# Kernel tuning notes

Measured on AMD Instinct MI355X. Metric: run time of the kernel, lower is better.

The kernel has to match this reference:

```python
import jax, jax.numpy as jnp
import numpy as np

NUM_EXPERTS = 8
CAPACITY_C = 1.0
ROUTER_TEMP = 1.0
EPS = 1e-10


def reference(x, router_w, router_b, w_gate, b_gate, w_up, b_up, w_down, b_down):
    # x: [B, S, H]
    B, S, H = x.shape
    n_tok = B * S
    k = int(n_tok * CAPACITY_C) // NUM_EXPERTS  # expert capacity (1024 here)

    xf = x.reshape(n_tok, H)  # (b s) h

    # Linear router (dropout p=0 -> identity), computed in float32 as in .float()
    clean_h = xf @ router_w + router_b  # [n_tok, E]

    # Gumbel noise (deterministic key stands in for torch.rand_like)
    u = jax.random.uniform(jax.random.key(42), clean_h.shape, dtype=clean_h.dtype)
    gumbel = -jnp.log(-jnp.log(u + EPS) + EPS)
    h = (clean_h + gumbel) / ROUTER_TEMP

    Sm = jax.nn.softmax(h, axis=-1)  # softmax over experts

    # top-k over the TOKEN dim (dim=0) per expert -> expert-choice routing
    Gt, idxt = jax.lax.top_k(Sm.T, k)  # [E, k]
    G = Gt.T            # [k, E] routing weights
    idx = idxt.T        # [k, E] chosen token indices

    # Gather routed tokens (replaces the one-hot einsum gather exactly:
    # top-k indices are distinct per expert, so one-hot matmul == take)
    toks = jnp.take(xf, idx, axis=0)  # [k, E, H]

    # Shared SwiGLU FFN (group_size=1 -> one expert instance reused E times)
    gate = jax.nn.silu(toks @ w_gate + b_gate)  # [k, E, dff]
    up = toks @ w_up + b_up                      # [k, E, dff]
    e_out = (gate * up) @ w_down + b_down        # [k, E, H]

    # Weight by G and scatter-add back to token positions, summed over experts
    weighted = G[..., None] * e_out              # [k, E, H]
    y = jnp.zeros_like(xf).at[idx.reshape(-1)].add(weighted.reshape(-1, H))
    return y.reshape(B, S, H)


def setup_inputs() -> dict:
    key = jax.random.key(0)
    ks = jax.random.split(key, 6)
    B, S, H, E = 4, 2048, 2048, NUM_EXPERTS
    dff = int(H * 4 * 2 / 3)  # 5461
    sH = 1.0 / np.sqrt(H)
    sF = 1.0 / np.sqrt(dff)
    return {
        "x": jax.random.normal(ks[0], (B, S, H), dtype=jnp.float32),
        "router_w": jax.random.normal(ks[1], (H, E), dtype=jnp.float32) * sH,
        "router_b": jnp.zeros((E,), dtype=jnp.float32),
        "w_gate": jax.random.normal(ks[2], (H, dff), dtype=jnp.float32) * sH,
        "b_gate": jnp.zeros((dff,), dtype=jnp.float32),
        "w_up": jax.random.normal(ks[3], (H, dff), dtype=jnp.float32) * sH,
        "b_up": jnp.zeros((dff,), dtype=jnp.float32),
        "w_down": jax.random.normal(ks[4], (dff, H), dtype=jnp.float32) * sF,
        "b_down": jnp.zeros((H,), dtype=jnp.float32),
    }
```

## Files before the change

### kernel.cpp

```cpp
#include <hip/hip_runtime.h>
#include <cstdint>
#include <cstddef>

#define N_TOK  8192
#define HDIM   2048
#define NEXP   8
#define KCAP   1024
#define DFF    5461
#define DFF_PB 5504
#define ACT_P  5504
#define NT1    (HDIM / 64)
#define NT2    (ACT_P / 64)

typedef unsigned short u16;
typedef short bf16x8 __attribute__((ext_vector_type(8)));
typedef float f32x4  __attribute__((ext_vector_type(4)));

__device__ __forceinline__ u16 f2bf(float f) {
  uint32_t u = __float_as_uint(f);
  uint32_t r = (u + 0x7FFFu + ((u >> 16) & 1u)) >> 16;
  return (u16)r;
}

__device__ __forceinline__ uint32_t rotl32(uint32_t v, int d) {
  return (v << d) | (v >> (32 - d));
}

__device__ uint32_t threefry_bits(uint32_t idx) {
  const uint32_t ks0 = 0u, ks1 = 42u, ks2 = 0u ^ 42u ^ 0x1BD11BDAu;
  uint32_t x0 = 0u + ks0;
  uint32_t x1 = idx + ks1;
#define TFR(d) { x0 += x1; x1 = rotl32(x1, d); x1 ^= x0; }
  TFR(13) TFR(15) TFR(26) TFR(6)
  x0 += ks1; x1 += ks2 + 1u;
  TFR(17) TFR(29) TFR(16) TFR(24)
  x0 += ks2; x1 += ks0 + 2u;
  TFR(13) TFR(15) TFR(26) TFR(6)
  x0 += ks0; x1 += ks1 + 3u;
  TFR(17) TFR(29) TFR(16) TFR(24)
  x0 += ks1; x1 += ks2 + 4u;
  TFR(13) TFR(15) TFR(26) TFR(6)
  x0 += ks2; x1 += ks0 + 5u;
#undef TFR
  return x0 ^ x1;
}

__global__ __launch_bounds__(256) void router_kernel(const float* __restrict__ x,
    const float* __restrict__ rw, const float* __restrict__ rb,
    float* __restrict__ SmT)
{
  const int lane = threadIdx.x & 63;
  const int wid  = threadIdx.x >> 6;
  const int t = blockIdx.x * 4 + wid;
  const float* xr = x + (size_t)t * HDIM;
  float acc[8] = {0.f,0.f,0.f,0.f,0.f,0.f,0.f,0.f};
#pragma unroll
  for (int it = 0; it < HDIM / 64; ++it) {
    int h = lane + it * 64;
    float xv = xr[h];
    const float4* wp = (const float4*)(rw + h * 8);
    float4 w0 = wp[0], w1 = wp[1];
    acc[0] = fmaf(xv, w0.x, acc[0]);
    acc[1] = fmaf(xv, w0.y, acc[1]);
    acc[2] = fmaf(xv, w0.z, acc[2]);
    acc[3] = fmaf(xv, w0.w, acc[3]);
    acc[4] = fmaf(xv, w1.x, acc[4]);
    acc[5] = fmaf(xv, w1.y, acc[5]);
    acc[6] = fmaf(xv, w1.z, acc[6]);
    acc[7] = fmaf(xv, w1.w, acc[7]);
  }
#pragma unroll
  for (int m = 32; m >= 1; m >>= 1) {
#pragma unroll
    for (int e = 0; e < 8; ++e) acc[e] += __shfl_xor(acc[e], m, 64);
  }
  if (lane == 0) {
    float h[8];
#pragma unroll
    for (int e = 0; e < 8; ++e) {
      uint32_t bits = threefry_bits((uint32_t)(t * 8 + e));
      float u = __uint_as_float((bits >> 9) | 0x3f800000u) - 1.0f;
      u = fmaxf(u, 0.0f);
      float g = -logf(-logf(u + 1e-10f) + 1e-10f);
      h[e] = acc[e] + rb[e] + g;
    }
    float mx = h[0];
#pragma unroll
    for (int e = 1; e < 8; ++e) mx = fmaxf(mx, h[e]);
    float ex[8]; float s = 0.f;
#pragma unroll
    for (int e = 0; e < 8; ++e) { ex[e] = expf(h[e] - mx); s += ex[e]; }
#pragma unroll
    for (int e = 0; e < 8; ++e) SmT[e * N_TOK + t] = ex[e] / s;
  }
}

__global__ __launch_bounds__(1024) void select_topk(const float* __restrict__ SmT,
    uint32_t* __restrict__ selTok, float* __restrict__ selW, int* __restrict__ inv)
{
  const int e = blockIdx.x;
  const int tid = threadIdx.x;
  const float* v = SmT + (size_t)e * N_TOK;
  __shared__ uint32_t hist[256];
  __shared__ uint32_t sh_byte, sh_kk, sh_cnt, sh_eqc;
  uint32_t bitsv[8];
#pragma unroll
  for (int i = 0; i < 8; ++i) bitsv[i] = __float_as_uint(v[tid + i * 1024]);
  uint32_t prefix = 0;
  uint32_t kk = KCAP;
  for (int s = 3; s >= 0; --s) {
    if (tid < 256) hist[tid] = 0;
    __syncthreads();
    uint32_t himask = (s == 3) ? 0u : (0xFFFFFFFFu << ((s + 1) * 8));
#pragma unroll
    for (int i = 0; i < 8; ++i) {
      uint32_t b = bitsv[i];
      if ((b & himask) == prefix) atomicAdd(&hist[(b >> (s * 8)) & 255u], 1u);
    }
    __syncthreads();
    if (tid == 0) {
      uint32_t cum = 0; uint32_t bsel = 0, kn = kk;
      for (int b = 255; b >= 0; --b) {
        uint32_t c = hist[b];
        if (cum + c >= kk) { bsel = (uint32_t)b; kn = kk - cum; break; }
        cum += c;
      }
      sh_byte = bsel; sh_kk = kn;
    }
    __syncthreads();
    prefix |= sh_byte << (s * 8);
    kk = sh_kk;
  }
  const uint32_t T = prefix;
  const uint32_t need = kk;
  if (tid == 0) { sh_cnt = 0; sh_eqc = 0; }
  __syncthreads();
#pragma unroll
  for (int i = 0; i < 8; ++i) {
    uint32_t b = bitsv[i];
    if (b > T) {
      uint32_t p = atomicAdd(&sh_cnt, 1u);
      const uint32_t tok = (uint32_t)(tid + i * 1024);
      selTok[e * KCAP + p] = tok;
      selW[e * KCAP + p] = __uint_as_float(b);
      inv[e * N_TOK + tok] = (int)(e * KCAP + p);
    } else if (b == T) {
      atomicAdd(&sh_eqc, 1u);
    }
  }
  __syncthreads();
  if (sh_eqc == need) {
#pragma unroll
    for (int i = 0; i < 8; ++i) {
      if (bitsv[i] == T) {
        uint32_t p = atomicAdd(&sh_cnt, 1u);
        const uint32_t tok = (uint32_t)(tid + i * 1024);
        selTok[e * KCAP + p] = tok;
        selW[e * KCAP + p] = __uint_as_float(T);
        inv[e * N_TOK + tok] = (int)(e * KCAP + p);
      }
    }
  } else if (tid == 0) {
    uint32_t p = sh_cnt, rem = need;
    for (int t = 0; t < N_TOK && rem > 0u; ++t) {
      if (__float_as_uint(v[t]) == T) {
        selTok[e * KCAP + p] = (uint32_t)t;
        selW[e * KCAP + p] = __uint_as_float(T);
        inv[e * N_TOK + t] = (int)(e * KCAP + p);
        ++p; --rem;
      }
    }
  }
}

__global__ __launch_bounds__(256) void gather_kernel(const float* __restrict__ x,
    const uint32_t* __restrict__ selTok, u16* __restrict__ Xsel)
{
  const int slot = blockIdx.x;
  const int tid = threadIdx.x;
  const uint32_t tok = selTok[slot];
  const float4* src = (const float4*)(x + (size_t)tok * HDIM);
  float4 a = src[tid * 2], b = src[tid * 2 + 1];
  union { u16 h[8]; uint4 vv; } pk;
  pk.h[0] = f2bf(a.x); pk.h[1] = f2bf(a.y); pk.h[2] = f2bf(a.z); pk.h[3] = f2bf(a.w);
  pk.h[4] = f2bf(b.x); pk.h[5] = f2bf(b.y); pk.h[6] = f2bf(b.z); pk.h[7] = f2bf(b.w);
  ((uint4*)(Xsel + (size_t)slot * HDIM))[tid] = pk.vv;
}

__global__ __launch_bounds__(256) void transpose_convert(const float* __restrict__ in,
    int rows_in, int cols_in, u16* __restrict__ out, int out_cols)
{
  __shared__ float tile[32][33];
  const int bi = blockIdx.y;
  const int bj = blockIdx.x;
  const int tx = threadIdx.x, ty = threadIdx.y;
#pragma unroll
  for (int t = 0; t < 4; ++t) {
    int r = bi * 32 + ty + t * 8, c = bj * 32 + tx;
    float vv = (r < rows_in && c < cols_in) ? in[(size_t)r * cols_in + c] : 0.0f;
    tile[ty + t * 8][tx] = vv;
  }
  __syncthreads();
#pragma unroll
  for (int t = 0; t < 4; ++t) {
    int oj = bj * 32 + ty + t * 8;
    int oi = bi * 32 + tx;
    out[(size_t)oj * out_cols + oi] = f2bf(tile[tx][ty + t * 8]);
  }
}

#if defined(__has_builtin)
#  if __has_builtin(__builtin_amdgcn_global_load_lds)
#    define HAVE_GLD 1
#  endif
#endif
#ifdef HAVE_GLD
#define STG(gp, lp) __builtin_amdgcn_global_load_lds( \
    (const __attribute__((address_space(1))) void*)(gp), \
    (__attribute__((address_space(3))) void*)(lp), 16, 0, 0)
#define WAITV6() asm volatile("s_waitcnt vmcnt(6)" ::: "memory")
#define WAITV4() asm volatile("s_waitcnt vmcnt(4)" ::: "memory")
#define WAITV2() asm volatile("s_waitcnt vmcnt(2)" ::: "memory")
#define WAITV0() asm volatile("s_waitcnt vmcnt(0)" ::: "memory")
#else
#define STG(gp, lp) (*(bf16x8*)(lp) = *(const bf16x8*)(gp))
#define WAITV6() asm volatile("s_waitcnt vmcnt(0) lgkmcnt(0)" ::: "memory")
#define WAITV4() asm volatile("s_waitcnt vmcnt(0) lgkmcnt(0)" ::: "memory")
#define WAITV2() asm volatile("s_waitcnt vmcnt(0) lgkmcnt(0)" ::: "memory")
#define WAITV0() asm volatile("s_waitcnt vmcnt(0) lgkmcnt(0)" ::: "memory")
#endif
#define WAITLGKM0() asm volatile("s_waitcnt lgkmcnt(0)" ::: "memory")
#define WAITLGKM8() asm volatile("s_waitcnt lgkmcnt(8)" ::: "memory")
#define BAR()    __builtin_amdgcn_s_barrier()
#define SCHED0() __builtin_amdgcn_sched_barrier(0)
#define PRIO1()  __builtin_amdgcn_s_setprio(1)
#define PRIO0()  __builtin_amdgcn_s_setprio(0)
#define MFMA(a, b, c) __builtin_amdgcn_mfma_f32_16x16x32_bf16(a, b, c, 0, 0, 0)


__global__ __launch_bounds__(512, 2) void gemm1_kernel(
    const u16* __restrict__ Xsel,
    const u16* __restrict__ WgT,
    const u16* __restrict__ WuT,
    const float* __restrict__ bg, const float* __restrict__ bu,
    u16* __restrict__ act)
{
  __shared__ u16 AL[2][2][8192];
  __shared__ u16 GL[2][8192];
  __shared__ u16 UL[2][8192];

  const int id = blockIdx.x;
  const int xcd = id & 7;
  const int r = id >> 3;
  const int bm = xcd * 4 + (r & 3);
  const int bn = r >> 2;

  const int tid = threadIdx.x;
  const int lane = tid & 63, wid = tid >> 6;
  const int wm = wid >> 2, wn = wid & 3;
  const int fr = lane & 15, ck = lane >> 4;
  const int sw0 = (ck ^ (fr & 7)) * 8;
  const int sw1 = sw0 ^ 32;
  const int rA = (wm * 64 + fr) * 64;
  const int rB = (wn * 32 + fr) * 64;

  const int sr = tid >> 3;
  const int sq = (tid & 7) ^ (sr & 7);
  const u16* aS0 = Xsel + (size_t)(bm * 256 + sr) * HDIM + sq * 8;
  const u16* aS1 = aS0 + (size_t)128 * HDIM;
  const u16* gS  = WgT + (size_t)(bn * 128 + sr) * HDIM + sq * 8;
  const u16* uS  = WuT + (size_t)(bn * 128 + sr) * HDIM + sq * 8;

#define ST_A0(kt) { u16* d = &AL[(kt)&1][0][tid*8]; \
    STG(aS0 + (kt)*64, d); STG(aS0 + (kt)*64 + (size_t)64*HDIM, d + 4096); }
#define ST_A1(kt) { u16* d = &AL[(kt)&1][1][tid*8]; \
    STG(aS1 + (kt)*64, d); STG(aS1 + (kt)*64 + (size_t)64*HDIM, d + 4096); }
#define ST_G(kt) { u16* d = &GL[(kt)&1][tid*8]; \
    STG(gS + (kt)*64, d); STG(gS + (kt)*64 + (size_t)64*HDIM, d + 4096); }
#define ST_U(kt) { u16* d = &UL[(kt)&1][tid*8]; \
    STG(uS + (kt)*64, d); STG(uS + (kt)*64 + (size_t)64*HDIM, d + 4096); }

  f32x4 accg[8][2], accu[8][2];
  const f32x4 z4 = {0.f, 0.f, 0.f, 0.f};
#pragma unroll
  for (int i = 0; i < 8; ++i)
#pragma unroll
    for (int n = 0; n < 2; ++n) { accg[i][n] = z4; accu[i][n] = z4; }

  bf16x8 af[4][2], bgf[2][2], buf[2][2];

  ST_A0(0) ST_G(0) ST_U(0) ST_A1(0)
  WAITV4(); BAR(); SCHED0();

  for (int kt = 0; kt < NT1; ++kt) {
    const u16* A0 = AL[kt & 1][0];
    const u16* A1 = AL[kt & 1][1];
    const u16* G  = GL[kt & 1];
    const u16* U  = UL[kt & 1];
    const int st = (kt + 1 < NT1);
#pragma unroll
    for (int i = 0; i < 4; ++i) {
      af[i][0] = *(const bf16x8*)&A0[rA + i * 1024 + sw0];
      af[i][1] = *(const bf16x8*)&A0[rA + i * 1024 + sw1];
    }
#pragma unroll
    for (int n = 0; n < 2; ++n) {
      bgf[n][0] = *(const bf16x8*)&G[rB + n * 1024 + sw0];
      bgf[n][1] = *(const bf16x8*)&G[rB + n * 1024 + sw1];
    }
    if (st) ST_A0(kt + 1)
    WAITLGKM8();
    BAR();
    WAITLGKM0(); SCHED0();
    PRIO1();
#pragma unroll
    for (int ks = 0; ks < 2; ++ks)
#pragma unroll
      for (int i = 0; i < 4; ++i)
#pragma unroll
        for (int n = 0; n < 2; ++n)
          accg[i][n] = MFMA(af[i][ks], bgf[n][ks], accg[i][n]);
    PRIO0();
    if (st) { WAITV4(); } else { WAITV2(); }
    BAR(); SCHED0();
#pragma unroll
    for (int n = 0; n < 2; ++n) {
      buf[n][0] = *(const bf16x8*)&U[rB + n * 1024 + sw0];
      buf[n][1] = *(const bf16x8*)&U[rB + n * 1024 + sw1];
    }
    if (st) { ST_G(kt + 1) ST_U(kt + 1) }
    BAR();
    WAITLGKM0(); SCHED0();
    PRIO1();
#pragma unroll
    for (int ks = 0; ks < 2; ++ks)
#pragma unroll
      for (int i = 0; i < 4; ++i)
#pragma unroll
        for (int n = 0; n < 2; ++n)
          accu[i][n] = MFMA(af[i][ks], buf[n][ks], accu[i][n]);
    PRIO0();
    if (st) { WAITV6(); } else { WAITV0(); }
    BAR(); SCHED0();
#pragma unroll
    for (int i = 0; i < 4; ++i) {
      af[i][0] = *(const bf16x8*)&A1[rA + i * 1024 + sw0];
      af[i][1] = *(const bf16x8*)&A1[rA + i * 1024 + sw1];
    }
    if (st) ST_A1(kt + 1)
    BAR();
    WAITLGKM0(); SCHED0();
    PRIO1();
#pragma unroll
    for (int ks = 0; ks < 2; ++ks)
#pragma unroll
      for (int i = 0; i < 4; ++i)
#pragma unroll
        for (int n = 0; n < 2; ++n) {
          accg[4 + i][n] = MFMA(af[i][ks], bgf[n][ks], accg[4 + i][n]);
          accu[4 + i][n] = MFMA(af[i][ks], buf[n][ks], accu[4 + i][n]);
        }
    PRIO0();
    WAITV4();
    BAR(); SCHED0();
  }

#pragma unroll
  for (int f = 0; f < 8; ++f) {
    const int rbase = bm * 256 + (f >> 2) * 128 + wm * 64 + (f & 3) * 16 + ck * 4;
#pragma unroll
    for (int v = 0; v < 4; ++v) {
      u16* arow = act + (size_t)(rbase + v) * ACT_P;
#pragma unroll
      for (int n = 0; n < 2; ++n) {
        const int col = bn * 128 + wn * 32 + n * 16 + fr;
        u16 ov = 0;
        if (col < DFF) {
          float gv = accg[f][n][v] + bg[col];
          float uv = accu[f][n][v] + bu[col];
          float e = __expf(-gv);
          float sv = gv * __builtin_amdgcn_rcpf(1.0f + e);
          ov = f2bf(sv * uv);
        }
        arow[col] = ov;
      }
    }
  }
#undef ST_A0
#undef ST_A1
#undef ST_G
#undef ST_U
}

__global__ __launch_bounds__(512, 2) void gemm2_kernel(
    const u16* __restrict__ act,
    const u16* __restrict__ WdT,
    const float* __restrict__ bd,
    const float* __restrict__ selW,
    float* __restrict__ Yslot)
{
  __shared__ u16 AL[2][2][8192];
  __shared__ u16 BL[2][2][8192];

  const int id = blockIdx.x;
  const int wg = (id & 7) * 32 + (id >> 3);
  const int bm = wg & 31, bn = wg >> 5;

  const int tid = threadIdx.x;
  const int lane = tid & 63, wid = tid >> 6;
  const int wm = wid >> 2, wn = wid & 3;
  const int fr = lane & 15, ck = lane >> 4;
  const int sw0 = (ck ^ (fr & 7)) * 8;
  const int sw1 = sw0 ^ 32;
  const int rA = (wm * 64 + fr) * 64;
  const int rB = (wn * 32 + fr) * 64;

  const int sr = tid >> 3;
  const int sq = (tid & 7) ^ (sr & 7);
  const u16* aS0 = act + (size_t)(bm * 256 + sr) * ACT_P + sq * 8;
  const u16* aS1 = aS0 + (size_t)128 * ACT_P;
  const u16* bS0 = WdT + (size_t)(bn * 256 + sr) * ACT_P + sq * 8;
  const u16* bS1 = bS0 + (size_t)128 * ACT_P;

#define ST_A0(kt) { u16* d = &AL[(kt)&1][0][tid*8]; \
    STG(aS0 + (kt)*64, d); STG(aS0 + (kt)*64 + (size_t)64*ACT_P, d + 4096); }
#define ST_A1(kt) { u16* d = &AL[(kt)&1][1][tid*8]; \
    STG(aS1 + (kt)*64, d); STG(aS1 + (kt)*64 + (size_t)64*ACT_P, d + 4096); }
#define ST_B0(kt) { u16* d = &BL[(kt)&1][0][tid*8]; \
    STG(bS0 + (kt)*64, d); STG(bS0 + (kt)*64 + (size_t)64*ACT_P, d + 4096); }
#define ST_B1(kt) { u16* d = &BL[(kt)&1][1][tid*8]; \
    STG(bS1 + (kt)*64, d); STG(bS1 + (kt)*64 + (size_t)64*ACT_P, d + 4096); }

  f32x4 acc[8][4];
  const f32x4 z4 = {0.f, 0.f, 0.f, 0.f};
#pragma unroll
  for (int i = 0; i < 8; ++i)
#pragma unroll
    for (int n = 0; n < 4; ++n) acc[i][n] = z4;

  bf16x8 af[4][2], b0[2][2], b1[2][2];

  ST_A0(0) ST_B0(0) ST_B1(0) ST_A1(0)
  WAITV4(); BAR(); SCHED0();

  for (int kt = 0; kt < NT2; ++kt) {
    const u16* A0 = AL[kt & 1][0];
    const u16* A1 = AL[kt & 1][1];
    const u16* B0 = BL[kt & 1][0];
    const u16* B1 = BL[kt & 1][1];
    const int st = (kt + 1 < NT2);
#pragma unroll
    for (int i = 0; i < 4; ++i) {
      af[i][0] = *(const bf16x8*)&A0[rA + i * 1024 + sw0];
      af[i][1] = *(const bf16x8*)&A0[rA + i * 1024 + sw1];
    }
#pragma unroll
    for (int n = 0; n < 2; ++n) {
      b0[n][0] = *(const bf16x8*)&B0[rB + n * 1024 + sw0];
      b0[n][1] = *(const bf16x8*)&B0[rB + n * 1024 + sw1];
    }
    if (st) ST_A0(kt + 1)
    WAITLGKM8();
    BAR();
    WAITLGKM0(); SCHED0();
    PRIO1();
#pragma unroll
    for (int ks = 0; ks < 2; ++ks)
#pragma unroll
      for (int i = 0; i < 4; ++i)
#pragma unroll
        for (int n = 0; n < 2; ++n)
          acc[i][n] = MFMA(af[i][ks], b0[n][ks], acc[i][n]);
    PRIO0();
    if (st) { WAITV4(); } else { WAITV2(); }
    BAR(); SCHED0();
#pragma unroll
    for (int n = 0; n < 2; ++n) {
      b1[n][0] = *(const bf16x8*)&B1[rB + n * 1024 + sw0];
      b1[n][1] = *(const bf16x8*)&B1[rB + n * 1024 + sw1];
    }
    if (st) { ST_B0(kt + 1) ST_B1(kt + 1) }
    BAR();
    WAITLGKM0(); SCHED0();
    PRIO1();
#pragma unroll
    for (int ks = 0; ks < 2; ++ks)
#pragma unroll
      for (int i = 0; i < 4; ++i)
#pragma unroll
        for (int n = 0; n < 2; ++n)
          acc[i][2 + n] = MFMA(af[i][ks], b1[n][ks], acc[i][2 + n]);
    PRIO0();
    if (st) { WAITV6(); } else { WAITV0(); }
    BAR(); SCHED0();
#pragma unroll
    for (int i = 0; i < 4; ++i) {
      af[i][0] = *(const bf16x8*)&A1[rA + i * 1024 + sw0];
      af[i][1] = *(const bf16x8*)&A1[rA + i * 1024 + sw1];
    }
    if (st) ST_A1(kt + 1)
    BAR();
    WAITLGKM0(); SCHED0();
    PRIO1();
#pragma unroll
    for (int ks = 0; ks < 2; ++ks)
#pragma unroll
      for (int i = 0; i < 4; ++i)
#pragma unroll
        for (int n = 0; n < 2; ++n) {
          acc[4 + i][n]     = MFMA(af[i][ks], b0[n][ks], acc[4 + i][n]);
          acc[4 + i][2 + n] = MFMA(af[i][ks], b1[n][ks], acc[4 + i][2 + n]);
        }
    PRIO0();
    WAITV4();
    BAR(); SCHED0();
  }

#pragma unroll
  for (int f = 0; f < 8; ++f) {
    const int rbase = bm * 256 + (f >> 2) * 128 + wm * 64 + (f & 3) * 16 + ck * 4;
#pragma unroll
    for (int v = 0; v < 4; ++v) {
      const int srow = rbase + v;
      const float w = selW[srow];
      float* yrow = Yslot + (size_t)srow * HDIM;
#pragma unroll
      for (int n = 0; n < 4; ++n) {
        const int col = bn * 256 + (n >> 1) * 128 + wn * 32 + (n & 1) * 16 + fr;
        yrow[col] = w * (acc[f][n][v] + bd[col]);
      }
    }
  }
#undef ST_A0
#undef ST_A1
#undef ST_B0
#undef ST_B1
}

__global__ __launch_bounds__(256) void scatter_kernel(const float* __restrict__ Yslot,
    const int* __restrict__ inv, float* __restrict__ y)
{
  const int t = blockIdx.x;
  const int c = threadIdx.x * 8;
  float4 a0 = {0.f,0.f,0.f,0.f}, a1 = {0.f,0.f,0.f,0.f};
#pragma unroll
  for (int e = 0; e < 8; ++e) {
    const int s = inv[e * N_TOK + t];
    if (s >= 0) {
      const float4* p = (const float4*)(Yslot + (size_t)s * HDIM + c);
      float4 v0 = p[0], v1 = p[1];
      a0.x += v0.x; a0.y += v0.y; a0.z += v0.z; a0.w += v0.w;
      a1.x += v1.x; a1.y += v1.y; a1.z += v1.z; a1.w += v1.w;
    }
  }
  float4* yp = (float4*)(y + (size_t)t * HDIM + c);
  yp[0] = a0; yp[1] = a1;
}

extern "C" void kernel_launch(void* const* d_in, const int* in_sizes, int n_in,
                              void* d_out, int out_size, void* d_ws, size_t ws_size,
                              hipStream_t stream) {
  const float* x      = (const float*)d_in[0];
  const float* rw     = (const float*)d_in[1];
  const float* rb     = (const float*)d_in[2];
  const float* w_gate = (const float*)d_in[3];
  const float* b_gate = (const float*)d_in[4];
  const float* w_up   = (const float*)d_in[5];
  const float* b_up   = (const float*)d_in[6];
  const float* w_down = (const float*)d_in[7];
  const float* b_down = (const float*)d_in[8];
  float* y = (float*)d_out;

  uint8_t* ws = (uint8_t*)d_ws;
  uint32_t* selTok = (uint32_t*)(ws + 0);
  float*    selW   = (float*)(ws + 32768);
  int*      inv    = (int*)(ws + 65536);
  u16*      act    = (u16*)(ws + 327680);
  u16*      Xsel   = (u16*)(ws + 90505216ull);
  u16*      WdT    = (u16*)(ws + 90505216ull);
  float*    Yslot  = (float*)(ws + 113049600ull);
  float*    SmT    = (float*)(ws + 124059648ull);
  u16*      WgT    = (u16*)(ws + 124321792ull);
  u16*      WuT    = (u16*)(ws + 146866176ull);

  hipMemsetAsync(inv, 0xFF, NEXP * N_TOK * sizeof(int), stream);
  transpose_convert<<<dim3(172, 64), dim3(32, 8), 0, stream>>>(w_gate, 2048, DFF, WgT, 2048);
  transpose_convert<<<dim3(172, 64), dim3(32, 8), 0, stream>>>(w_up,   2048, DFF, WuT, 2048);
  router_kernel<<<N_TOK / 4, 256, 0, stream>>>(x, rw, rb, SmT);
  select_topk<<<NEXP, 1024, 0, stream>>>(SmT, selTok, selW, inv);
  gather_kernel<<<N_TOK, 256, 0, stream>>>(x, selTok, Xsel);
  gemm1_kernel<<<43 * 32, 512, 0, stream>>>(Xsel, WgT, WuT, b_gate, b_up, act);
  transpose_convert<<<dim3(64, 172), dim3(32, 8), 0, stream>>>(w_down, DFF, 2048, WdT, ACT_P);
  gemm2_kernel<<<8 * 32, 512, 0, stream>>>(act, WdT, b_down, selW, Yslot);
  scatter_kernel<<<N_TOK, 256, 0, stream>>>(Yslot, inv, y);
}
```

Baseline: 891.4 us.

## Drop mid-tile barriers in GEMM loops and merge gate/up weight transposes

Removes the barrier and LDS-wait pairs placed between issuing the next tile's global-to-LDS stores and the MFMA blocks in both GEMM kernels, leaving only the trailing barrier per phase. It also merges the two gate/up weight transpose launches into one grid with a z dimension. The intent is to cut synchronisation stalls and one launch. The risk is that MFMAs may now rely on compiler-inserted lgkmcnt waits, and a wave may overwrite a buffer another wave is still reading.

```diff
diff --git a/kernel.cpp b/kernel.cpp
--- a/kernel.cpp
+++ b/kernel.cpp
@@ -206,6 +206,31 @@
     int oj = bj * 32 + ty + t * 8;
     int oi = bi * 32 + tx;
     out[(size_t)oj * out_cols + oi] = f2bf(tile[tx][ty + t * 8]);
+  }
+}
+
+__global__ __launch_bounds__(256) void transpose_convert_gu(
+    const float* __restrict__ g, const float* __restrict__ u,
+    u16* __restrict__ og, u16* __restrict__ ou)
+{
+  const float* in = blockIdx.z ? u : g;
+  u16* out = blockIdx.z ? ou : og;
+  __shared__ float tile[32][33];
+  const int bi = blockIdx.y;
+  const int bj = blockIdx.x;
+  const int tx = threadIdx.x, ty = threadIdx.y;
+#pragma unroll
+  for (int t = 0; t < 4; ++t) {
+    int r = bi * 32 + ty + t * 8, c = bj * 32 + tx;
+    float vv = (r < 2048 && c < DFF) ? in[(size_t)r * DFF + c] : 0.0f;
+    tile[ty + t * 8][tx] = vv;
+  }
+  __syncthreads();
+#pragma unroll
+  for (int t = 0; t < 4; ++t) {
+    int oj = bj * 32 + ty + t * 8;
+    int oi = bi * 32 + tx;
+    out[(size_t)oj * 2048 + oi] = f2bf(tile[tx][ty + t * 8]);
   }
 }
 
@@ -229,8 +254,6 @@
 #define WAITV2() asm volatile("s_waitcnt vmcnt(0) lgkmcnt(0)" ::: "memory")
 #define WAITV0() asm volatile("s_waitcnt vmcnt(0) lgkmcnt(0)" ::: "memory")
 #endif
-#define WAITLGKM0() asm volatile("s_waitcnt lgkmcnt(0)" ::: "memory")
-#define WAITLGKM8() asm volatile("s_waitcnt lgkmcnt(8)" ::: "memory")
 #define BAR()    __builtin_amdgcn_s_barrier()
 #define SCHED0() __builtin_amdgcn_sched_barrier(0)
 #define PRIO1()  __builtin_amdgcn_s_setprio(1)
@@ -309,9 +332,6 @@
       bgf[n][1] = *(const bf16x8*)&G[rB + n * 1024 + sw1];
     }
     if (st) ST_A0(kt + 1)
-    WAITLGKM8();
-    BAR();
-    WAITLGKM0(); SCHED0();
     PRIO1();
 #pragma unroll
     for (int ks = 0; ks < 2; ++ks)
@@ -329,8 +349,6 @@
       buf[n][1] = *(const bf16x8*)&U[rB + n * 1024 + sw1];
     }
     if (st) { ST_G(kt + 1) ST_U(kt + 1) }
-    BAR();
-    WAITLGKM0(); SCHED0();
     PRIO1();
 #pragma unroll
     for (int ks = 0; ks < 2; ++ks)
@@ -348,8 +366,6 @@
       af[i][1] = *(const bf16x8*)&A1[rA + i * 1024 + sw1];
     }
     if (st) ST_A1(kt + 1)
-    BAR();
-    WAITLGKM0(); SCHED0();
     PRIO1();
 #pragma unroll
     for (int ks = 0; ks < 2; ++ks)
@@ -460,9 +476,6 @@
       b0[n][1] = *(const bf16x8*)&B0[rB + n * 1024 + sw1];
     }
     if (st) ST_A0(kt + 1)
-    WAITLGKM8();
-    BAR();
-    WAITLGKM0(); SCHED0();
     PRIO1();
 #pragma unroll
     for (int ks = 0; ks < 2; ++ks)
@@ -480,8 +493,6 @@
       b1[n][1] = *(const bf16x8*)&B1[rB + n * 1024 + sw1];
     }
     if (st) { ST_B0(kt + 1) ST_B1(kt + 1) }
-    BAR();
-    WAITLGKM0(); SCHED0();
     PRIO1();
 #pragma unroll
     for (int ks = 0; ks < 2; ++ks)
@@ -499,8 +510,6 @@
       af[i][1] = *(const bf16x8*)&A1[rA + i * 1024 + sw1];
     }
     if (st) ST_A1(kt + 1)
-    BAR();
-    WAITLGKM0(); SCHED0();
     PRIO1();
 #pragma unroll
     for (int ks = 0; ks < 2; ++ks)
@@ -584,8 +593,7 @@
   u16*      WuT    = (u16*)(ws + 146866176ull);
 
   hipMemsetAsync(inv, 0xFF, NEXP * N_TOK * sizeof(int), stream);
-  transpose_convert<<<dim3(172, 64), dim3(32, 8), 0, stream>>>(w_gate, 2048, DFF, WgT, 2048);
-  transpose_convert<<<dim3(172, 64), dim3(32, 8), 0, stream>>>(w_up,   2048, DFF, WuT, 2048);
+  transpose_convert_gu<<<dim3(172, 64, 2), dim3(32, 8), 0, stream>>>(w_gate, w_up, WgT, WuT);
   router_kernel<<<N_TOK / 4, 256, 0, stream>>>(x, rw, rb, SmT);
   select_topk<<<NEXP, 1024, 0, stream>>>(SmT, selTok, selW, inv);
   gather_kernel<<<N_TOK, 256, 0, stream>>>(x, selTok, Xsel);
```

New measurement: 867.4 us. -2.7%, faster.
